# Optimization experiments

Measured on AMD Instinct MI355X. Metric: run time of the kernel, lower is better.

Reference implementation:

```python
import jax, jax.numpy as jnp
from jax import lax
import numpy as np

B = 8192   # samples
L = 32     # predicted chars per sample (num_chars[i])
M = 32     # target labels per sample (num_labels[i])
C = 96     # character classes


def _edit_trace(pred, tgt):
    """Levenshtein DP + backtrace for one sample.
    pred: [L] int, tgt: [M] int.
    Returns (ti, tj, valid) of length L+M: 1-based (i,j) positions of the
    diagonal (match/substitute) moves on the optimal edit path, as emitted by
    distance_and_trace; valid masks non-diagonal / out-of-path steps."""
    Ls, Ms = pred.shape[0], tgt.shape[0]
    cost = (pred[:, None] != tgt[None, :]).astype(jnp.int32)  # [L,M]
    row0 = jnp.arange(Ms + 1, dtype=jnp.int32)

    def row_step(prev, crow):
        first = prev[0] + 1
        def col_step(left, z):
            up, diag, c = z
            v = jnp.minimum(jnp.minimum(up + 1, left + 1), diag + c)
            return v, v
        _, rest = lax.scan(col_step, first, (prev[1:], prev[:-1], crow))
        new = jnp.concatenate([first[None], rest])
        return new, new

    _, rows = lax.scan(row_step, row0, cost)
    D = jnp.concatenate([row0[None, :], rows], axis=0)  # [L+1, M+1]

    def bt_step(carry, _):
        i, j = carry
        c = cost[jnp.maximum(i - 1, 0), jnp.maximum(j - 1, 0)]
        dij = D[i, j]
        diag = (i > 0) & (j > 0) & (D[i - 1, j - 1] + c == dij)
        up = (~diag) & (i > 0) & (D[i - 1, j] + 1 == dij)
        left = (~diag) & (~up) & (j > 0)
        ni = i - (diag | up).astype(jnp.int32)
        nj = j - (diag | left).astype(jnp.int32)
        return (ni, nj), (i, j, diag)

    (_, _), (ti, tj, valid) = lax.scan(
        bt_step, (jnp.int32(Ls), jnp.int32(Ms)), None, length=Ls + Ms)
    return ti, tj, valid


def _forward(x, y, num_chars, num_labels):
    b = num_chars.shape[0]
    c = x.shape[1]
    l = x.shape[0] // b
    m = y.shape[0] // b
    logits = x.reshape(b, l, c)          # [B,L,C]
    labels = y.reshape(b, m)             # [B,M]
    pred = jnp.argmax(logits, axis=-1)   # torch.max(x,1) indices
    ti, tj, valid = jax.vmap(_edit_trace)(pred, labels)  # [B, L+M] each
    logp = jax.nn.log_softmax(logits, axis=-1)
    xi = jnp.where(valid, ti - 1, 0)     # trace[:,0]-1 (+ per-sample offset via reshape)
    yi = jnp.where(valid, tj - 1, 0)     # trace[:,1]-1
    lab = jnp.take_along_axis(labels, yi, axis=1)                 # [B,L+M]
    lp = jnp.take_along_axis(logp, xi[..., None], axis=1)         # [B,L+M,C]
    ce = -jnp.take_along_axis(lp, lab[..., None], axis=2)[..., 0]  # [B,L+M]
    cnt = valid.sum(axis=1)
    per_sample = jnp.where(valid, ce, 0.0).sum(axis=1) / jnp.maximum(cnt, 1)
    nonempty = cnt > 0                   # attenuation: skip empty traces
    total = jnp.where(nonempty, per_sample, 0.0).sum()
    return total / nonempty.sum()


def setup_inputs() -> dict:
    key = jax.random.key(0)
    k1, k2 = jax.random.split(key)
    x = jax.random.normal(k1, (B * L, C), dtype=jnp.float32)
    y = jax.random.randint(k2, (B * M,), 0, C, dtype=jnp.int32)
    num_chars = jnp.full((B,), L, dtype=jnp.int32)
    num_labels = jnp.full((B,), M, dtype=jnp.int32)
    return {"x": x, "y": y, "num_chars": num_chars, "num_labels": num_labels}


def reference(x, y, num_chars, num_labels):
    return _forward(x, y, num_chars, num_labels)
```

## Files before the change

### kernel.cpp

```cpp
#include <hip/hip_runtime.h>
#include <hip/hip_bf16.h>
#include <stdint.h>

#define BNUM  8192
#define LROWS 32
#define MLAB  32
#define CCLS  96
#define WPB   4
#define SPW   2
#define SPB   (WPB*SPW)
#define NBLK  (BNUM/SPB)

__global__ __launch_bounds__(256) void editloss_main(
    const float* __restrict__ x, const int* __restrict__ y,
    float* __restrict__ partial_sum, float* __restrict__ partial_cnt)
{
    __shared__ float ceTab[SPB][LROWS * MLAB];
    __shared__ float psum[SPB];
    __shared__ float pcnt[SPB];

    const int w    = threadIdx.x >> 6;
    const int lane = threadIdx.x & 63;
    const int g    = lane >> 5;
    const int u    = lane & 31;
    const int s    = w * SPW + g;
    const int sb   = blockIdx.x * SPB + s;

    const float* xs    = x + (size_t)sb * (LROWS * CCLS);
    const int    lab_u = y[sb * MLAB + u];

    for (int r = 0; r < LROWS; ++r) {
        const float* row = xs + r * CCLS;
        const float v0 = row[u * 3 + 0];
        const float v1 = row[u * 3 + 1];
        const float v2 = row[u * 3 + 2];
        const float xg = row[lab_u];
        float m = fmaxf(fmaxf(v0, v1), v2);
#pragma unroll
        for (int t = 16; t >= 1; t >>= 1) m = fmaxf(m, __shfl_xor(m, t));
        int cand = (v0 == m) ? (u * 3)
                 : (v1 == m) ? (u * 3 + 1)
                 : (v2 == m) ? (u * 3 + 2) : 4096;
#pragma unroll
        for (int t = 16; t >= 1; t >>= 1) cand = min(cand, __shfl_xor(cand, t));
        float se = __expf(v0 - m) + __expf(v1 - m) + __expf(v2 - m);
#pragma unroll
        for (int t = 16; t >= 1; t >>= 1) se += __shfl_xor(se, t);
        const float lse = m + __logf(se);
        const float ce  = lse - xg;
        ceTab[s][r * MLAB + u] = (cand == lab_u) ? ce : -ce;
    }
    __syncthreads();

    const int j = u + 1;
    int   prevW = 0;   float prevCE = 0.f;
    int   diagW = 0;   float diagCE = 0.f;
    for (int d = 1; d <= LROWS + MLAB; ++d) {
        const int   lWs  = __shfl_up(prevW, 1);
        const float lCEs = __shfl_up(prevCE, 1);
        const int i = d - j;
        const int   lW  = (u == 0) ? max(i, 0)     : lWs;
        const float lCE = (u == 0) ? 0.f           : lCEs;
        const int   dW  = (u == 0) ? max(i - 1, 0) : diagW;
        const float dCE = (u == 0) ? 0.f           : diagCE;
        int curW; float curCE;
        if (i <= 0) {
            curW = j; curCE = 0.f;
        } else if (i > LROWS) {
            curW = prevW; curCE = prevCE;
        } else {
            const int uD = prevW & 255, uC = prevW >> 8;
            const int lD = lW & 255,    lC = lW >> 8;
            const int dD = dW & 255,    dC = dW >> 8;
            const float ct  = ceTab[s][(i - 1) * MLAB + (j - 1)];
            const int   c   = (ct < 0.f) ? 1 : 0;
            const float cev = fabsf(ct);
            const int nD = min(min(uD, lD) + 1, dD + c);
            const bool dg = (dD + c == nD);
            const bool up = !dg && (uD + 1 == nD);
            int nC; float nCE;
            if (dg)      { nC = dC + 1; nCE = dCE + cev; }
            else if (up) { nC = uC;     nCE = prevCE;    }
            else         { nC = lC;     nCE = lCE;       }
            curW = nD | (nC << 8);
            curCE = nCE;
        }
        diagW = lWs; diagCE = lCEs;
        prevW = curW; prevCE = curCE;
    }

    if (u == 31) {
        const int cnt = prevW >> 8;
        psum[s] = (cnt > 0) ? prevCE / (float)cnt : 0.f;
        pcnt[s] = (cnt > 0) ? 1.f : 0.f;
    }
    __syncthreads();
    if (threadIdx.x == 0) {
        float ss = 0.f, cc = 0.f;
#pragma unroll
        for (int k = 0; k < SPB; ++k) { ss += psum[k]; cc += pcnt[k]; }
        partial_sum[blockIdx.x] = ss;
        partial_cnt[blockIdx.x] = cc;
    }
}

__global__ __launch_bounds__(256) void editloss_finalize(
    const float* __restrict__ partial_sum, const float* __restrict__ partial_cnt,
    float* __restrict__ out, int nblocks)
{
    float s = 0.f, c = 0.f;
    for (int k = threadIdx.x; k < nblocks; k += 256) {
        s += partial_sum[k];
        c += partial_cnt[k];
    }
#pragma unroll
    for (int d = 32; d >= 1; d >>= 1) {
        s += __shfl_xor(s, d);
        c += __shfl_xor(c, d);
    }
    __shared__ float ss[4], cc[4];
    const int w = threadIdx.x >> 6, lane = threadIdx.x & 63;
    if (lane == 0) { ss[w] = s; cc[w] = c; }
    __syncthreads();
    if (threadIdx.x == 0) {
        const float S  = ss[0] + ss[1] + ss[2] + ss[3];
        const float C2 = cc[0] + cc[1] + cc[2] + cc[3];
        out[0] = (C2 > 0.f) ? (S / C2) : 0.f;
    }
}

extern "C" void kernel_launch(void* const* d_in, const int* in_sizes, int n_in,
                              void* d_out, int out_size, void* d_ws, size_t ws_size,
                              hipStream_t stream) {
    const float* x = (const float*)d_in[0];
    const int*   y = (const int*)d_in[1];
    float* out = (float*)d_out;

    float* partial_sum = (float*)d_ws;
    float* partial_cnt = partial_sum + NBLK;

    editloss_main<<<NBLK, 256, 0, stream>>>(x, y, partial_sum, partial_cnt);
    editloss_finalize<<<1, 256, 0, stream>>>(partial_sum, partial_cnt, out, NBLK);
}
```

Baseline: 176.3 us.

## Use DPP cross-lane reductions and branchless packed-key DP wavefront

Replaces shfl_xor/shfl_up with DPP row moves plus a ds_swizzle for the 32-lane reductions and the wavefront shift. Drops the __syncthreads between the cost-table fill and the DP, since each 32-lane group only reads its own table slice. Drops max-subtraction in the softmax, encodes the DP min/tie-break as one packed integer key with a branchless select, and fully unrolls the diagonal loop. Skipping the max-subtraction risks exp overflow for large logits, and the DP now relies on implicit intra-wave ordering of LDS writes and reads.

```diff
diff --git a/kernel.cpp b/kernel.cpp
--- a/kernel.cpp
+++ b/kernel.cpp
@@ -1,5 +1,4 @@
 #include <hip/hip_runtime.h>
-#include <hip/hip_bf16.h>
 #include <stdint.h>
 
 #define BNUM  8192
@@ -11,7 +10,48 @@
 #define SPB   (WPB*SPW)
 #define NBLK  (BNUM/SPB)
 
-__global__ __launch_bounds__(256) void editloss_main(
+#define CTL_XOR1  0xB1
+#define CTL_XOR2  0x4E
+#define CTL_HMIR  0x141
+#define CTL_MIR   0x140
+#define CTL_SHR1  0x138
+#define SWZ_XOR16 0x401F
+
+template <int CTL>
+__device__ __forceinline__ int dppmov(int v) {
+    return __builtin_amdgcn_update_dpp(v, v, CTL, 0xF, 0xF, false);
+}
+
+__device__ __forceinline__ float red_max32(float v) {
+    v = fmaxf(v, __int_as_float(dppmov<CTL_XOR1>(__float_as_int(v))));
+    v = fmaxf(v, __int_as_float(dppmov<CTL_XOR2>(__float_as_int(v))));
+    v = fmaxf(v, __int_as_float(dppmov<CTL_HMIR>(__float_as_int(v))));
+    v = fmaxf(v, __int_as_float(dppmov<CTL_MIR >(__float_as_int(v))));
+    v = fmaxf(v, __int_as_float(__builtin_amdgcn_ds_swizzle(__float_as_int(v), SWZ_XOR16)));
+    return v;
+}
+__device__ __forceinline__ float red_add32(float v) {
+    v += __int_as_float(dppmov<CTL_XOR1>(__float_as_int(v)));
+    v += __int_as_float(dppmov<CTL_XOR2>(__float_as_int(v)));
+    v += __int_as_float(dppmov<CTL_HMIR>(__float_as_int(v)));
+    v += __int_as_float(dppmov<CTL_MIR >(__float_as_int(v)));
+    v += __int_as_float(__builtin_amdgcn_ds_swizzle(__float_as_int(v), SWZ_XOR16));
+    return v;
+}
+__device__ __forceinline__ int red_min32(int v) {
+    v = min(v, dppmov<CTL_XOR1>(v));
+    v = min(v, dppmov<CTL_XOR2>(v));
+    v = min(v, dppmov<CTL_HMIR>(v));
+    v = min(v, dppmov<CTL_MIR >(v));
+    v = min(v, __builtin_amdgcn_ds_swizzle(v, SWZ_XOR16));
+    return v;
+}
+__device__ __forceinline__ int   shr1_i(int v)   { return dppmov<CTL_SHR1>(v); }
+__device__ __forceinline__ float shr1_f(float v) {
+    return __int_as_float(dppmov<CTL_SHR1>(__float_as_int(v)));
+}
+
+__global__ __launch_bounds__(256, 4) void editloss_main(
     const float* __restrict__ x, const int* __restrict__ y,
     float* __restrict__ partial_sum, float* __restrict__ partial_cnt)
 {
@@ -29,76 +69,71 @@
     const float* xs    = x + (size_t)sb * (LROWS * CCLS);
     const int    lab_u = y[sb * MLAB + u];
 
+#pragma unroll 2
     for (int r = 0; r < LROWS; ++r) {
         const float* row = xs + r * CCLS;
         const float v0 = row[u * 3 + 0];
         const float v1 = row[u * 3 + 1];
         const float v2 = row[u * 3 + 2];
         const float xg = row[lab_u];
-        float m = fmaxf(fmaxf(v0, v1), v2);
-#pragma unroll
-        for (int t = 16; t >= 1; t >>= 1) m = fmaxf(m, __shfl_xor(m, t));
+        float m = red_max32(fmaxf(fmaxf(v0, v1), v2));
         int cand = (v0 == m) ? (u * 3)
                  : (v1 == m) ? (u * 3 + 1)
                  : (v2 == m) ? (u * 3 + 2) : 4096;
-#pragma unroll
-        for (int t = 16; t >= 1; t >>= 1) cand = min(cand, __shfl_xor(cand, t));
-        float se = __expf(v0 - m) + __expf(v1 - m) + __expf(v2 - m);
-#pragma unroll
-        for (int t = 16; t >= 1; t >>= 1) se += __shfl_xor(se, t);
-        const float lse = m + __logf(se);
+        cand = red_min32(cand);
+        const float se  = red_add32(__expf(v0) + __expf(v1) + __expf(v2));
+        const float lse = __logf(se);
         const float ce  = lse - xg;
         ceTab[s][r * MLAB + u] = (cand == lab_u) ? ce : -ce;
     }
-    __syncthreads();
 
     const int j = u + 1;
-    int   prevW = 0;   float prevCE = 0.f;
-    int   diagW = 0;   float diagCE = 0.f;
+    int prevD = 0, prevC = 0; float prevCE = 0.f;
+    int diagD = 0, diagC = 0; float diagCE = 0.f;
+#pragma unroll
     for (int d = 1; d <= LROWS + MLAB; ++d) {
-        const int   lWs  = __shfl_up(prevW, 1);
-        const float lCEs = __shfl_up(prevCE, 1);
+        const int   lDs  = shr1_i(prevD);
+        const int   lCs  = shr1_i(prevC);
+        const float lCEs = shr1_f(prevCE);
         const int i = d - j;
-        const int   lW  = (u == 0) ? max(i, 0)     : lWs;
-        const float lCE = (u == 0) ? 0.f           : lCEs;
-        const int   dW  = (u == 0) ? max(i - 1, 0) : diagW;
-        const float dCE = (u == 0) ? 0.f           : diagCE;
-        int curW; float curCE;
-        if (i <= 0) {
-            curW = j; curCE = 0.f;
-        } else if (i > LROWS) {
-            curW = prevW; curCE = prevCE;
-        } else {
-            const int uD = prevW & 255, uC = prevW >> 8;
-            const int lD = lW & 255,    lC = lW >> 8;
-            const int dD = dW & 255,    dC = dW >> 8;
-            const float ct  = ceTab[s][(i - 1) * MLAB + (j - 1)];
-            const int   c   = (ct < 0.f) ? 1 : 0;
-            const float cev = fabsf(ct);
-            const int nD = min(min(uD, lD) + 1, dD + c);
-            const bool dg = (dD + c == nD);
-            const bool up = !dg && (uD + 1 == nD);
-            int nC; float nCE;
-            if (dg)      { nC = dC + 1; nCE = dCE + cev; }
-            else if (up) { nC = uC;     nCE = prevCE;    }
-            else         { nC = lC;     nCE = lCE;       }
-            curW = nD | (nC << 8);
-            curCE = nCE;
-        }
-        diagW = lWs; diagCE = lCEs;
-        prevW = curW; prevCE = curCE;
+        const int   lD  = (u == 0) ? ((i > 0) ? i : 0)     : lDs;
+        const int   lC  = (u == 0) ? 0                     : lCs;
+        const float lCE = (u == 0) ? 0.f                   : lCEs;
+        const int   dD  = (u == 0) ? ((i > 1) ? i - 1 : 0) : diagD;
+        const int   dC  = (u == 0) ? 0                     : diagC;
+        const float dCE = (u == 0) ? 0.f                   : diagCE;
+
+        const int rc = min(max(i - 1, 0), LROWS - 1);
+        const float ct = ceTab[s][rc * MLAB + u];
+        const int c4 = (int)((__float_as_uint(ct) >> 29) & 4u);
+
+        const int ku = prevD * 4 + 5;
+        const int kl = lD   * 4 + 6;
+        const int kd = dD   * 4 + c4;
+        const int k  = min(min(ku, kl), kd);
+        const int pr = k & 3;
+        const int nD = k >> 2;
+        const int   nC  = (pr == 0) ? dC + 1          : ((pr == 1) ? prevC  : lC);
+        const float nCE = (pr == 0) ? dCE + fabsf(ct) : ((pr == 1) ? prevCE : lCE);
+
+        int curD; int curC; float curCE;
+        if (i <= 0)          { curD = j;     curC = 0;     curCE = 0.f;    }
+        else if (i > LROWS)  { curD = prevD; curC = prevC; curCE = prevCE; }
+        else                 { curD = nD;    curC = nC;    curCE = nCE;    }
+
+        diagD = lDs; diagC = lCs; diagCE = lCEs;
+        prevD = curD; prevC = curC; prevCE = curCE;
     }
 
     if (u == 31) {
-        const int cnt = prevW >> 8;
-        psum[s] = (cnt > 0) ? prevCE / (float)cnt : 0.f;
-        pcnt[s] = (cnt > 0) ? 1.f : 0.f;
+        psum[s] = (prevC > 0) ? prevCE / (float)prevC : 0.f;
+        pcnt[s] = (prevC > 0) ? 1.f : 0.f;
     }
     __syncthreads();
     if (threadIdx.x == 0) {
         float ss = 0.f, cc = 0.f;
 #pragma unroll
-        for (int k = 0; k < SPB; ++k) { ss += psum[k]; cc += pcnt[k]; }
+        for (int kk = 0; kk < SPB; ++kk) { ss += psum[kk]; cc += pcnt[kk]; }
         partial_sum[blockIdx.x] = ss;
         partial_cnt[blockIdx.x] = cc;
     }
```

New measurement: 173.3 us. About the same (-1.7%).
